# Optimization experiments

Hardware: AMD Instinct MI355X
Metric: run time of the kernel (lower is better)

## Reference

```python
import jax, jax.numpy as jnp
from jax import lax
import numpy as np


def setup_inputs() -> dict:
    key = jax.random.key(0)
    k1, k2, k3 = jax.random.split(key, 3)
    B, C, H, W = 4, 64, 512, 512
    K1, K2 = 5, 4
    x = jax.random.normal(k1, (B, C, H, W), dtype=jnp.float32)
    # matches nn.init.uniform_(w, 0.1, 0.2)
    conv1_weight = jax.random.uniform(k2, (C, 1, K1), dtype=jnp.float32, minval=0.1, maxval=0.2)
    conv2_weight = jax.random.uniform(k3, (C, K2 - 1), dtype=jnp.float32, minval=0.1, maxval=0.2)
    return {"x": x, "conv1_weight": conv1_weight, "conv2_weight": conv2_weight}


def _iir_conv2d_l2r(x, conv1_weight, conv2_weight):
    B, C, H, W = x.shape
    K2m1 = conv2_weight.shape[1]  # number of feedback taps = conv2_window - 1
    # (B,C,H,W) -> (B*H, C, W): each row is an independent 1D signal
    r = jnp.transpose(x, (0, 2, 1, 3)).reshape(B * H, C, W)
    # FIR stage: depthwise conv1d, 'same' padding, groups=C
    f = lax.conv_general_dilated(
        r, conv1_weight,
        window_strides=(1,), padding='SAME',
        dimension_numbers=('NCH', 'OIH', 'NCH'),
        feature_group_count=C)
    # IIR stage: y[j] = f[j] - sum_{t=0}^{K2m1-1} w[:,t] * y[j - K2m1 + t]
    # (weight index 0 multiplies the oldest output, index K2m1-1 the most recent)
    def step(carry, f_j):
        # carry: (BH, C, K2m1) last K2m1 outputs, oldest first; f_j: (BH, C)
        y = f_j - jnp.einsum('rct,ct->rc', carry, conv2_weight)
        carry = jnp.concatenate([carry[:, :, 1:], y[:, :, None]], axis=2)
        return carry, y

    init = jnp.zeros((B * H, C, K2m1), dtype=f.dtype)  # zero left-padding
    _, ys = lax.scan(step, init, jnp.moveaxis(f, 2, 0))  # ys: (W, BH, C)
    y = jnp.moveaxis(ys, 0, 2).reshape(B, H, C, W)       # (B,H,C,W)
    return jnp.transpose(y, (0, 2, 1, 3))                # (B,C,H,W)


def reference(x, conv1_weight, conv2_weight):
    # direction = LEFT2RIGHT: no flip/transpose pre/post
    return _iir_conv2d_l2r(x, conv1_weight, conv2_weight)
```

## Files before the change

### kernel.cpp

```cpp
#include <hip/hip_runtime.h>


constexpr int Wd    = 512;
constexpr int TROWS = 8;
constexpr int NT    = 256;
constexpr int F4ROW = Wd / 4;

__global__ __launch_bounds__(NT, 6)
void iir_conv2d_kernel(const float4* __restrict__ x4,
                       const float* __restrict__ w1,
                       const float* __restrict__ w2,
                       float4* __restrict__ y4)
{
    const int tid  = threadIdx.x;
    const int lane = tid & 63;
    const int r    = tid >> 5;
    const int s    = tid & 31;
    const int row0 = blockIdx.x * TROWS;
    const int row  = row0 + r;
    const int c    = (row0 >> 9) & 63;

    const float a0 = w1[c*5+0], a1 = w1[c*5+1], a2 = w1[c*5+2],
                a3 = w1[c*5+3], a4 = w1[c*5+4];
    const float v0 = w2[c*3+0], v1 = w2[c*3+1], v2 = w2[c*3+2];

    const float4* __restrict__ xr = x4 + (size_t)row * F4ROW;
    float4 xv0 = xr[4*s+0], xv1 = xr[4*s+1], xv2 = xr[4*s+2], xv3 = xr[4*s+3];

    float M[3][3];
    {
        float h3a = 1.f, h2a = 0.f, h1a = 0.f;
        float h3b = 0.f, h2b = 1.f, h1b = 0.f;
        float h3c = 0.f, h2c = 0.f, h1c = 1.f;
        #pragma unroll
        for (int k = 0; k < 16; ++k) {
            const float na = -(v0*h3a + v1*h2a + v2*h1a);
            const float nb = -(v0*h3b + v1*h2b + v2*h1b);
            const float nc = -(v0*h3c + v1*h2c + v2*h1c);
            if (k == 13) { M[0][0] = na; M[0][1] = nb; M[0][2] = nc; }
            if (k == 14) { M[1][0] = na; M[1][1] = nb; M[1][2] = nc; }
            if (k == 15) { M[2][0] = na; M[2][1] = nb; M[2][2] = nc; }
            h3a = h2a; h2a = h1a; h1a = na;
            h3b = h2b; h2b = h1b; h1b = nb;
            h3c = h2c; h2c = h1c; h1c = nc;
        }
    }

    float xw[24];
    {
        const int srcL = (s >= 1)  ? (lane - 1) : lane;
        const int srcR = (s <= 30) ? (lane + 1) : lane;
        float l0 = __shfl(xv3.x, srcL, 64);
        float l1 = __shfl(xv3.y, srcL, 64);
        float l2 = __shfl(xv3.z, srcL, 64);
        float l3 = __shfl(xv3.w, srcL, 64);
        float r0 = __shfl(xv0.x, srcR, 64);
        float r1 = __shfl(xv0.y, srcR, 64);
        float r2 = __shfl(xv0.z, srcR, 64);
        float r3 = __shfl(xv0.w, srcR, 64);
        if (s == 0)  { l0 = 0.f; l1 = 0.f; l2 = 0.f; l3 = 0.f; }
        if (s == 31) { r0 = 0.f; r1 = 0.f; r2 = 0.f; r3 = 0.f; }
        xw[0]=l0;  xw[1]=l1;  xw[2]=l2;  xw[3]=l3;
        xw[4]=xv0.x;  xw[5]=xv0.y;  xw[6]=xv0.z;  xw[7]=xv0.w;
        xw[8]=xv1.x;  xw[9]=xv1.y;  xw[10]=xv1.z; xw[11]=xv1.w;
        xw[12]=xv2.x; xw[13]=xv2.y; xw[14]=xv2.z; xw[15]=xv2.w;
        xw[16]=xv3.x; xw[17]=xv3.y; xw[18]=xv3.z; xw[19]=xv3.w;
        xw[20]=r0; xw[21]=r1; xw[22]=r2; xw[23]=r3;
    }

    float y[16];
    {
        float ym3 = 0.f, ym2 = 0.f, ym1 = 0.f;
        #pragma unroll
        for (int k = 0; k < 16; ++k) {
            const float f = a0*xw[k+2] + a1*xw[k+3] + a2*xw[k+4]
                          + a3*xw[k+5] + a4*xw[k+6];
            const float t = v0*ym3 + v1*ym2;
            const float yy = (f - t) - v2*ym1;
            y[k] = yy;
            ym3 = ym2; ym2 = ym1; ym1 = yy;
        }
    }

    float b0 = y[13], b1 = y[14], b2 = y[15];
    #pragma unroll
    for (int rd = 0; rd < 5; ++rd) {
        const int d = 1 << rd;
        const int src = (s >= d) ? (lane - d) : lane;
        const float g0 = __shfl(b0, src, 64);
        const float g1 = __shfl(b1, src, 64);
        const float g2 = __shfl(b2, src, 64);
        if (s >= d) {
            b0 += M[0][0]*g0 + M[0][1]*g1 + M[0][2]*g2;
            b1 += M[1][0]*g0 + M[1][1]*g1 + M[1][2]*g2;
            b2 += M[2][0]*g0 + M[2][1]*g1 + M[2][2]*g2;
        }
        if (rd < 4) {
            float N[3][3];
            #pragma unroll
            for (int i = 0; i < 3; ++i)
                #pragma unroll
                for (int j = 0; j < 3; ++j)
                    N[i][j] = M[i][0]*M[0][j] + M[i][1]*M[1][j] + M[i][2]*M[2][j];
            #pragma unroll
            for (int i = 0; i < 3; ++i)
                #pragma unroll
                for (int j = 0; j < 3; ++j) M[i][j] = N[i][j];
        }
    }

    {
        const int src = (s >= 1) ? (lane - 1) : lane;
        float wm3 = __shfl(b0, src, 64);
        float wm2 = __shfl(b1, src, 64);
        float wm1 = __shfl(b2, src, 64);
        if (s == 0) { wm3 = 0.f; wm2 = 0.f; wm1 = 0.f; }
        #pragma unroll
        for (int k = 0; k < 16; ++k) {
            const float w = -(v0*wm3 + v1*wm2 + v2*wm1);
            y[k] += w;
            wm3 = wm2; wm2 = wm1; wm1 = w;
        }
    }

    float4* __restrict__ yrow = y4 + (size_t)row * F4ROW;
    #pragma unroll
    for (int u = 0; u < 4; ++u) {
        const int srcl = (lane & 32) | (8*u + ((lane & 31) >> 2));
        float out0, out1, out2, out3;
        #pragma unroll
        for (int q = 0; q < 4; ++q) {
            const float t0 = __shfl(y[4*q+0], srcl, 64);
            const float t1 = __shfl(y[4*q+1], srcl, 64);
            const float t2 = __shfl(y[4*q+2], srcl, 64);
            const float t3 = __shfl(y[4*q+3], srcl, 64);
            if ((lane & 3) == q) { out0 = t0; out1 = t1; out2 = t2; out3 = t3; }
        }
        float4 o; o.x = out0; o.y = out1; o.z = out2; o.w = out3;
        yrow[32*u + (lane & 31)] = o;
    }
}

extern "C" void kernel_launch(void* const* d_in, const int* in_sizes, int n_in,
                              void* d_out, int out_size, void* d_ws, size_t ws_size,
                              hipStream_t stream) {
    const float4* x4 = (const float4*)d_in[0];
    const float*  w1 = (const float*)d_in[1];
    const float*  w2 = (const float*)d_in[2];
    float4* y4 = (float4*)d_out;

    const int nrows  = out_size / Wd;
    const int blocks = nrows / TROWS;
    iir_conv2d_kernel<<<blocks, NT, 0, stream>>>(x4, w1, w2, y4);
}
```

Measured before the change: 104.5 us.

## Map one row per wavefront with 8-element chunks and shared scan matrices

Each 512-wide row is now handled by a full 64-lane wavefront with 8 elements per lane, where before half a wavefront handled a row with 16 elements per lane. The scan gains a sixth round. The 3x3 transfer-matrix powers are computed once per block by thread 0 and stored in shared memory, replacing the per-thread matrix squaring inside the scan loop. This shortens per-thread serial recurrences, cuts register use so more blocks fit per CU, and removes redundant matrix multiplies. The cost is an added __syncthreads, a serial setup step on one thread, and an extra shuffle round.

Result: slower. 117.9 us (+12.8%).

```diff
diff --git a/kernel.cpp b/kernel.cpp
--- a/kernel.cpp
+++ b/kernel.cpp
@@ -2,22 +2,24 @@
 
 
 constexpr int Wd    = 512;
-constexpr int TROWS = 8;
+constexpr int TROWS = 4;
 constexpr int NT    = 256;
 constexpr int F4ROW = Wd / 4;
 
-__global__ __launch_bounds__(NT, 6)
+__global__ __launch_bounds__(NT, 8)
 void iir_conv2d_kernel(const float4* __restrict__ x4,
                        const float* __restrict__ w1,
                        const float* __restrict__ w2,
                        float4* __restrict__ y4)
 {
+    __shared__ float Mt[6][9];
+
     const int tid  = threadIdx.x;
     const int lane = tid & 63;
-    const int r    = tid >> 5;
-    const int s    = tid & 31;
+    const int wv   = tid >> 6;
+    const int s    = lane;
     const int row0 = blockIdx.x * TROWS;
-    const int row  = row0 + r;
+    const int row  = row0 + wv;
     const int c    = (row0 >> 9) & 63;
 
     const float a0 = w1[c*5+0], a1 = w1[c*5+1], a2 = w1[c*5+2],
@@ -25,56 +27,63 @@
     const float v0 = w2[c*3+0], v1 = w2[c*3+1], v2 = w2[c*3+2];
 
     const float4* __restrict__ xr = x4 + (size_t)row * F4ROW;
-    float4 xv0 = xr[4*s+0], xv1 = xr[4*s+1], xv2 = xr[4*s+2], xv3 = xr[4*s+3];
+    float4 xv0 = xr[2*s+0], xv1 = xr[2*s+1];
 
-    float M[3][3];
-    {
+    if (tid == 0) {
         float h3a = 1.f, h2a = 0.f, h1a = 0.f;
         float h3b = 0.f, h2b = 1.f, h1b = 0.f;
         float h3c = 0.f, h2c = 0.f, h1c = 1.f;
+        float P[9];
         #pragma unroll
-        for (int k = 0; k < 16; ++k) {
+        for (int k = 0; k < 8; ++k) {
             const float na = -(v0*h3a + v1*h2a + v2*h1a);
             const float nb = -(v0*h3b + v1*h2b + v2*h1b);
             const float nc = -(v0*h3c + v1*h2c + v2*h1c);
-            if (k == 13) { M[0][0] = na; M[0][1] = nb; M[0][2] = nc; }
-            if (k == 14) { M[1][0] = na; M[1][1] = nb; M[1][2] = nc; }
-            if (k == 15) { M[2][0] = na; M[2][1] = nb; M[2][2] = nc; }
+            if (k == 5) { P[0] = na; P[1] = nb; P[2] = nc; }
+            if (k == 6) { P[3] = na; P[4] = nb; P[5] = nc; }
+            if (k == 7) { P[6] = na; P[7] = nb; P[8] = nc; }
             h3a = h2a; h2a = h1a; h1a = na;
             h3b = h2b; h2b = h1b; h1b = nb;
             h3c = h2c; h2c = h1c; h1c = nc;
         }
+        #pragma unroll
+        for (int j = 0; j < 9; ++j) Mt[0][j] = P[j];
+        #pragma unroll
+        for (int rd = 1; rd < 6; ++rd) {
+            float N[9];
+            #pragma unroll
+            for (int i = 0; i < 3; ++i)
+                #pragma unroll
+                for (int j = 0; j < 3; ++j)
+                    N[3*i+j] = P[3*i+0]*P[0+j] + P[3*i+1]*P[3+j] + P[3*i+2]*P[6+j];
+            #pragma unroll
+            for (int j = 0; j < 9; ++j) { Mt[rd][j] = N[j]; P[j] = N[j]; }
+        }
     }
 
-    float xw[24];
+    float xw[12];
     {
         const int srcL = (s >= 1)  ? (lane - 1) : lane;
-        const int srcR = (s <= 30) ? (lane + 1) : lane;
-        float l0 = __shfl(xv3.x, srcL, 64);
-        float l1 = __shfl(xv3.y, srcL, 64);
-        float l2 = __shfl(xv3.z, srcL, 64);
-        float l3 = __shfl(xv3.w, srcL, 64);
+        const int srcR = (s <= 62) ? (lane + 1) : lane;
+        float l2 = __shfl(xv1.z, srcL, 64);
+        float l3 = __shfl(xv1.w, srcL, 64);
         float r0 = __shfl(xv0.x, srcR, 64);
         float r1 = __shfl(xv0.y, srcR, 64);
-        float r2 = __shfl(xv0.z, srcR, 64);
-        float r3 = __shfl(xv0.w, srcR, 64);
-        if (s == 0)  { l0 = 0.f; l1 = 0.f; l2 = 0.f; l3 = 0.f; }
-        if (s == 31) { r0 = 0.f; r1 = 0.f; r2 = 0.f; r3 = 0.f; }
-        xw[0]=l0;  xw[1]=l1;  xw[2]=l2;  xw[3]=l3;
-        xw[4]=xv0.x;  xw[5]=xv0.y;  xw[6]=xv0.z;  xw[7]=xv0.w;
-        xw[8]=xv1.x;  xw[9]=xv1.y;  xw[10]=xv1.z; xw[11]=xv1.w;
-        xw[12]=xv2.x; xw[13]=xv2.y; xw[14]=xv2.z; xw[15]=xv2.w;
-        xw[16]=xv3.x; xw[17]=xv3.y; xw[18]=xv3.z; xw[19]=xv3.w;
-        xw[20]=r0; xw[21]=r1; xw[22]=r2; xw[23]=r3;
+        if (s == 0)  { l2 = 0.f; l3 = 0.f; }
+        if (s == 63) { r0 = 0.f; r1 = 0.f; }
+        xw[0] = l2; xw[1] = l3;
+        xw[2] = xv0.x; xw[3] = xv0.y; xw[4]  = xv0.z; xw[5]  = xv0.w;
+        xw[6] = xv1.x; xw[7] = xv1.y; xw[8]  = xv1.z; xw[9]  = xv1.w;
+        xw[10] = r0; xw[11] = r1;
     }
 
-    float y[16];
+    float y[8];
     {
         float ym3 = 0.f, ym2 = 0.f, ym1 = 0.f;
         #pragma unroll
-        for (int k = 0; k < 16; ++k) {
-            const float f = a0*xw[k+2] + a1*xw[k+3] + a2*xw[k+4]
-                          + a3*xw[k+5] + a4*xw[k+6];
+        for (int k = 0; k < 8; ++k) {
+            const float f = a0*xw[k] + a1*xw[k+1] + a2*xw[k+2]
+                          + a3*xw[k+3] + a4*xw[k+4];
             const float t = v0*ym3 + v1*ym2;
             const float yy = (f - t) - v2*ym1;
             y[k] = yy;
@@ -82,30 +91,23 @@
         }
     }
 
-    float b0 = y[13], b1 = y[14], b2 = y[15];
+    __syncthreads();
+
+    float b0 = y[5], b1 = y[6], b2 = y[7];
     #pragma unroll
-    for (int rd = 0; rd < 5; ++rd) {
+    for (int rd = 0; rd < 6; ++rd) {
         const int d = 1 << rd;
+        const float m00 = Mt[rd][0], m01 = Mt[rd][1], m02 = Mt[rd][2];
+        const float m10 = Mt[rd][3], m11 = Mt[rd][4], m12 = Mt[rd][5];
+        const float m20 = Mt[rd][6], m21 = Mt[rd][7], m22 = Mt[rd][8];
         const int src = (s >= d) ? (lane - d) : lane;
         const float g0 = __shfl(b0, src, 64);
         const float g1 = __shfl(b1, src, 64);
         const float g2 = __shfl(b2, src, 64);
         if (s >= d) {
-            b0 += M[0][0]*g0 + M[0][1]*g1 + M[0][2]*g2;
-            b1 += M[1][0]*g0 + M[1][1]*g1 + M[1][2]*g2;
-            b2 += M[2][0]*g0 + M[2][1]*g1 + M[2][2]*g2;
-        }
-        if (rd < 4) {
-            float N[3][3];
-            #pragma unroll
-            for (int i = 0; i < 3; ++i)
-                #pragma unroll
-                for (int j = 0; j < 3; ++j)
-                    N[i][j] = M[i][0]*M[0][j] + M[i][1]*M[1][j] + M[i][2]*M[2][j];
-            #pragma unroll
-            for (int i = 0; i < 3; ++i)
-                #pragma unroll
-                for (int j = 0; j < 3; ++j) M[i][j] = N[i][j];
+            b0 += m00*g0 + m01*g1 + m02*g2;
+            b1 += m10*g0 + m11*g1 + m12*g2;
+            b2 += m20*g0 + m21*g1 + m22*g2;
         }
     }
 
@@ -116,7 +118,7 @@
         float wm1 = __shfl(b2, src, 64);
         if (s == 0) { wm3 = 0.f; wm2 = 0.f; wm1 = 0.f; }
         #pragma unroll
-        for (int k = 0; k < 16; ++k) {
+        for (int k = 0; k < 8; ++k) {
             const float w = -(v0*wm3 + v1*wm2 + v2*wm1);
             y[k] += w;
             wm3 = wm2; wm2 = wm1; wm1 = w;
@@ -125,19 +127,19 @@
 
     float4* __restrict__ yrow = y4 + (size_t)row * F4ROW;
     #pragma unroll
-    for (int u = 0; u < 4; ++u) {
-        const int srcl = (lane & 32) | (8*u + ((lane & 31) >> 2));
+    for (int u = 0; u < 2; ++u) {
+        const int srcl = 32*u + (lane >> 1);
         float out0, out1, out2, out3;
         #pragma unroll
-        for (int q = 0; q < 4; ++q) {
+        for (int q = 0; q < 2; ++q) {
             const float t0 = __shfl(y[4*q+0], srcl, 64);
             const float t1 = __shfl(y[4*q+1], srcl, 64);
             const float t2 = __shfl(y[4*q+2], srcl, 64);
             const float t3 = __shfl(y[4*q+3], srcl, 64);
-            if ((lane & 3) == q) { out0 = t0; out1 = t1; out2 = t2; out3 = t3; }
+            if ((lane & 1) == q) { out0 = t0; out1 = t1; out2 = t2; out3 = t3; }
         }
         float4 o; o.x = out0; o.y = out1; o.z = out2; o.w = out3;
-        yrow[32*u + (lane & 31)] = o;
+        yrow[64*u + lane] = o;
     }
 }
 
```
